# Optimization experiments

Hardware: AMD Instinct MI355X
Metric: run time of the kernel (lower is better)

The kernel has to match this reference:

```python
import jax, jax.numpy as jnp
import numpy as np

TOPK = 8
NUM_EXPERTS = 64


def setup_inputs() -> dict:
    key = jax.random.key(0)
    k0, k1, k2, k3 = jax.random.split(key, 4)
    B, S, H, E = 4, 4096, 2048, NUM_EXPERTS
    scale = (2.0 ** -0.5) * np.sqrt(6.0 / (H + E))  # xavier_uniform gain 2^-0.5
    return {
        "x": jax.random.normal(k0, (B, S, H), dtype=jnp.float32),
        "w_transform": jax.random.uniform(k1, (E, H), jnp.float32, -scale, scale),
        "w_noise": jax.random.uniform(k2, (E, H), jnp.float32, -scale, scale),
        "noise": jax.random.normal(k3, (E,), dtype=jnp.float32),
    }


def reference(x, w_transform, w_noise, noise):
    # weight: [B, S, E]
    logits_t = jnp.einsum("bsh,eh->bse", x, w_transform)
    logits_n = jnp.einsum("bsh,eh->bse", x, w_noise)
    weight = logits_t + jax.nn.softplus(logits_n) * noise  # broadcast noise [E]

    # Global (corpus-level) top-k over expert means
    mean_w = weight.mean(axis=(0, 1))  # [E]
    gates, indexes = jax.lax.top_k(mean_w, TOPK)
    selected_gates = jax.nn.softmax(gates, axis=-1)  # [TOPK]

    # Example-wise top-k -> multi-hot mask [B, S, E]
    _, ew_idx = jax.lax.top_k(weight, TOPK)  # [B, S, TOPK]
    mask = jax.nn.one_hot(ew_idx, NUM_EXPERTS, dtype=weight.dtype).sum(axis=-2) > 0

    # Masked softmax over experts
    masked = jnp.where(mask, weight, -jnp.inf)
    soft_w = jax.nn.softmax(masked, axis=-1)  # [B, S, E]

    # Experts balance loss: (std / mean)^2 of per-expert total weight
    sum_w = soft_w.sum(axis=(0, 1))  # [E]
    cv = jnp.std(sum_w, ddof=1) / jnp.mean(sum_w)  # torch .std() is unbiased
    balance_loss = cv ** 2

    return selected_gates, indexes, balance_loss
```

## Files before the change

### kernel.cpp

```cpp
#include <hip/hip_runtime.h>
#include <math.h>

#define H     2048
#define NE    64
#define KTOP  8
#define NTOK  16384
#define TOKB  64
#define STEPS 32

typedef __attribute__((ext_vector_type(8))) __bf16 bf16x8;
typedef __attribute__((ext_vector_type(8))) unsigned short us8;
typedef __attribute__((ext_vector_type(4))) float f32x4;

__device__ __forceinline__ unsigned short f2bf(float f) {
    unsigned u = __builtin_bit_cast(unsigned, f);
    return (unsigned short)((u + 0x7FFFu + ((u >> 16) & 1u)) >> 16);
}

#define GLOAD_F4(dst, ptr, OFF)                                        \
    asm volatile("global_load_dwordx4 %0, %1, off offset:%2"           \
                 : "=v"(dst) : "v"(ptr), "i"(OFF))
#define WAITV(N)                                                       \
    do { asm volatile("s_waitcnt vmcnt(%0)" :: "i"(N));                \
         __builtin_amdgcn_sched_barrier(0); } while (0)

__global__ __launch_bounds__(256) void k_prep(const float* __restrict__ Wt,
                                              const float* __restrict__ Wn,
                                              unsigned short* __restrict__ wbf2,
                                              float* __restrict__ sums) {
    const int gid = blockIdx.x * 256 + threadIdx.x;
    if (blockIdx.x == 0 && threadIdx.x < 128) sums[threadIdx.x] = 0.f;

    const int ln  = gid & 63;
    const int nb  = (gid >> 6) & 7;
    const int k32 = gid >> 9;
    const int row = nb * 16 + (ln & 15);
    const int col = k32 * 32 + (ln >> 4) * 8;
    const float* src = (row < NE) ? (Wt + (size_t)row * H + col)
                                  : (Wn + (size_t)(row - NE) * H + col);
    float4 v0 = *(const float4*)src;
    float4 v1 = *(const float4*)(src + 4);
    us8 o;
    o[0] = f2bf(v0.x); o[1] = f2bf(v0.y); o[2] = f2bf(v0.z); o[3] = f2bf(v0.w);
    o[4] = f2bf(v1.x); o[5] = f2bf(v1.y); o[6] = f2bf(v1.z); o[7] = f2bf(v1.w);
    *(us8*)(wbf2 + (size_t)gid * 8) = o;
}

__global__ __launch_bounds__(512, 2) void k_main(const float* __restrict__ X,
                                                 const unsigned short* __restrict__ wbf2,
                                                 const float* __restrict__ noise,
                                                 float* __restrict__ sumraw,
                                                 float* __restrict__ sumsoft) {
    __shared__ float cb[4][2048];
    __shared__ float epf[TOKB * 68];
    __shared__ float lsoft[NE];

    const int tid  = threadIdx.x;
    const int wid  = tid >> 6;
    const int lane = tid & 63;
    const int wm   = wid & 3;
    const int kp   = wid >> 2;
    const int lr   = lane & 15;
    const int lg   = lane >> 4;
    const int t0   = blockIdx.x * TOKB;
    const int s0   = (blockIdx.x >> 3) & 31;

    if (tid < NE) lsoft[tid] = 0.f;

    const float* xp = X + (size_t)(t0 + wm * 16 + lr) * H + kp * 1024 + lg * 8;
    const unsigned short* bp0 = wbf2 + (size_t)kp * 32 * 4096 + (size_t)lane * 8;

    f32x4 acc[8];
    #pragma unroll
    for (int i = 0; i < 8; ++i) acc[i] = (f32x4){0.f, 0.f, 0.f, 0.f};

    float4 xb[3][2];
    us8    bb[3][8];

    #define ISSUE(slot, sv)                                                  \
        do {                                                                 \
            const unsigned short* bA = bp0 + (size_t)(sv) * 4096;            \
            const unsigned short* bB = bA + 2048;                            \
            GLOAD_F4(bb[slot][0], bA, 0);                                    \
            GLOAD_F4(bb[slot][1], bA, 1024);                                 \
            GLOAD_F4(bb[slot][2], bA, 2048);                                 \
            GLOAD_F4(bb[slot][3], bA, 3072);                                 \
            GLOAD_F4(bb[slot][4], bB, 0);                                    \
            GLOAD_F4(bb[slot][5], bB, 1024);                                 \
            GLOAD_F4(bb[slot][6], bB, 2048);                                 \
            GLOAD_F4(bb[slot][7], bB, 3072);                                 \
            const float* xA = xp + (size_t)(sv) * 32;                        \
            GLOAD_F4(xb[slot][0], xA, 0);                                    \
            GLOAD_F4(xb[slot][1], xA, 16);                                   \
        } while (0)

    ISSUE(0, (s0 + 0) & 31);
    ISSUE(1, (s0 + 1) & 31);
    ISSUE(2, (s0 + 2) & 31);

    #pragma unroll
    for (int j = 0; j < STEPS; ++j) {
        const int slot = j % 3;
        if (j < STEPS - 2)       WAITV(20);
        else if (j == STEPS - 2) WAITV(10);
        else                     WAITV(0);

        float4 c0 = xb[slot][0], c1 = xb[slot][1];
        bf16x8 af;
        af[0] = (__bf16)c0.x; af[1] = (__bf16)c0.y;
        af[2] = (__bf16)c0.z; af[3] = (__bf16)c0.w;
        af[4] = (__bf16)c1.x; af[5] = (__bf16)c1.y;
        af[6] = (__bf16)c1.z; af[7] = (__bf16)c1.w;
        #pragma unroll
        for (int nb = 0; nb < 8; ++nb) {
            bf16x8 bfr = __builtin_bit_cast(bf16x8, bb[slot][nb]);
            acc[nb] = __builtin_amdgcn_mfma_f32_16x16x32_bf16(af, bfr, acc[nb], 0, 0, 0);
        }
        if (j + 3 < STEPS) ISSUE(slot, (s0 + j + 3) & 31);
    }
    #undef ISSUE

    if (kp == 1) {
        #pragma unroll
        for (int nb = 0; nb < 8; ++nb)
            #pragma unroll
            for (int r = 0; r < 4; ++r)
                cb[wm][(nb * 4 + r) * 64 + lane] = acc[nb][r];
    }
    __syncthreads();

    if (kp == 0) {
        #pragma unroll
        for (int nb = 0; nb < 8; ++nb)
            #pragma unroll
            for (int r = 0; r < 4; ++r)
                acc[nb][r] += cb[wm][(nb * 4 + r) * 64 + lane];
        float nz[4];
        #pragma unroll
        for (int nb = 0; nb < 4; ++nb) nz[nb] = noise[nb * 16 + lr];
        #pragma unroll
        for (int nb = 0; nb < 4; ++nb)
            #pragma unroll
            for (int r = 0; r < 4; ++r) {
                float lt  = acc[nb][r];
                float lnv = acc[nb + 4][r];
                float sp  = fmaxf(lnv, 0.f) + log1pf(expf(-fabsf(lnv)));
                epf[(wm * 16 + lg * 4 + r) * 68 + nb * 16 + lr] = lt + sp * nz[nb];
            }
    }
    __syncthreads();

    if (tid < TOKB) {
        float tv[KTOP]; int ti[KTOP];
        #pragma unroll
        for (int q = 0; q < KTOP; ++q) { tv[q] = -INFINITY; ti[q] = 0; }
        for (int e = 0; e < NE; ++e) {
            float cv = epf[tid * 68 + e]; int ci = e;
            #pragma unroll
            for (int q = 0; q < KTOP; ++q) {
                if (cv > tv[q]) {
                    float t_ = tv[q]; int i_ = ti[q];
                    tv[q] = cv; ti[q] = ci;
                    cv = t_; ci = i_;
                }
            }
        }
        float m = tv[0], den = 0.f, pr[KTOP];
        #pragma unroll
        for (int q = 0; q < KTOP; ++q) { pr[q] = expf(tv[q] - m); den += pr[q]; }
        float inv = 1.f / den;
        #pragma unroll
        for (int q = 0; q < KTOP; ++q) atomicAdd(&lsoft[ti[q]], pr[q] * inv);
    }
    __syncthreads();

    if (tid < NE) {
        float s = 0.f;
        #pragma unroll
        for (int t = 0; t < TOKB; ++t) s += epf[t * 68 + tid];
        atomicAdd(&sumraw[tid], s);
        atomicAdd(&sumsoft[tid], lsoft[tid]);
    }
}

__global__ void k_final(const float* __restrict__ sumraw,
                        const float* __restrict__ sumsoft,
                        float* __restrict__ out) {
    if (threadIdx.x != 0 || blockIdx.x != 0) return;

    float mw[NE];
    for (int e = 0; e < NE; ++e) mw[e] = sumraw[e] * (1.f / (float)NTOK);

    float tv[KTOP]; int ti[KTOP];
    for (int q = 0; q < KTOP; ++q) { tv[q] = -INFINITY; ti[q] = 0; }
    for (int e = 0; e < NE; ++e) {
        float cv = mw[e]; int ci = e;
        for (int q = 0; q < KTOP; ++q) {
            if (cv > tv[q]) {
                float t_ = tv[q]; int i_ = ti[q];
                tv[q] = cv; ti[q] = ci;
                cv = t_; ci = i_;
            }
        }
    }
    float m = tv[0], den = 0.f, pr[KTOP];
    for (int q = 0; q < KTOP; ++q) { pr[q] = expf(tv[q] - m); den += pr[q]; }
    for (int q = 0; q < KTOP; ++q) {
        out[q] = pr[q] / den;
        out[KTOP + q] = (float)ti[q];
    }

    float s = 0.f;
    for (int e = 0; e < NE; ++e) s += sumsoft[e];
    float mean = s / (float)NE;
    float var = 0.f;
    for (int e = 0; e < NE; ++e) { float d = sumsoft[e] - mean; var += d * d; }
    var /= (float)(NE - 1);
    out[16] = var / (mean * mean);
}

extern "C" void kernel_launch(void* const* d_in, const int* in_sizes, int n_in,
                              void* d_out, int out_size, void* d_ws, size_t ws_size,
                              hipStream_t stream) {
    (void)in_sizes; (void)n_in; (void)out_size; (void)ws_size;
    const float* x     = (const float*)d_in[0];
    const float* wt    = (const float*)d_in[1];
    const float* wn    = (const float*)d_in[2];
    const float* noise = (const float*)d_in[3];
    float* out = (float*)d_out;

    float* sumraw  = (float*)d_ws;
    float* sumsoft = sumraw + NE;
    unsigned short* wbf2 = (unsigned short*)(sumsoft + NE);

    k_prep<<<128, 256, 0, stream>>>(wt, wn, wbf2, sumraw);
    k_main<<<256, 512, 0, stream>>>(x, wbf2, noise, sumraw, sumsoft);
    k_final<<<1, 64, 0, stream>>>(sumraw, sumsoft, out);
}
```

Measured before the change: 93.77 us.

## Split experts across block pairs, widen token tile, move top-k to separate kernel

Each main block now computes 128 tokens but only half of the 128 output columns (transform or noise half), so each wave does two M-tiles against four B fragments. This halves the per-wave B loads and doubles A reuse. Logits are written to global memory as bf16, and a new k_topk kernel does softplus, noise mixing, per-token top-k and the reductions, one thread per token. The cost is an extra launch, a logits round trip through memory, bf16 rounding of the logits, and each X row being read by two blocks.

```diff
diff --git a/kernel.cpp b/kernel.cpp
--- a/kernel.cpp
+++ b/kernel.cpp
@@ -5,7 +5,7 @@
 #define NE    64
 #define KTOP  8
 #define NTOK  16384
-#define TOKB  64
+#define TOKB  128
 #define STEPS 32
 
 typedef __attribute__((ext_vector_type(8))) __bf16 bf16x8;
@@ -15,6 +15,9 @@
 __device__ __forceinline__ unsigned short f2bf(float f) {
     unsigned u = __builtin_bit_cast(unsigned, f);
     return (unsigned short)((u + 0x7FFFu + ((u >> 16) & 1u)) >> 16);
+}
+__device__ __forceinline__ float bf2f(unsigned short s) {
+    return __builtin_bit_cast(float, (unsigned)s << 16);
 }
 
 #define GLOAD_F4(dst, ptr, OFF)                                        \
@@ -26,34 +29,31 @@
 
 __global__ __launch_bounds__(256) void k_prep(const float* __restrict__ Wt,
                                               const float* __restrict__ Wn,
-                                              unsigned short* __restrict__ wbf2,
+                                              unsigned short* __restrict__ wbf3,
                                               float* __restrict__ sums) {
     const int gid = blockIdx.x * 256 + threadIdx.x;
     if (blockIdx.x == 0 && threadIdx.x < 128) sums[threadIdx.x] = 0.f;
 
-    const int ln  = gid & 63;
-    const int nb  = (gid >> 6) & 7;
-    const int k32 = gid >> 9;
-    const int row = nb * 16 + (ln & 15);
-    const int col = k32 * 32 + (ln >> 4) * 8;
-    const float* src = (row < NE) ? (Wt + (size_t)row * H + col)
-                                  : (Wn + (size_t)(row - NE) * H + col);
+    const int ln   = gid & 63;
+    const int nb   = (gid >> 6) & 3;
+    const int k32g = (gid >> 8) & 63;
+    const int h    = (gid >> 14) & 1;
+    const int c    = h * 64 + nb * 16 + (ln & 15);
+    const int col  = k32g * 32 + (ln >> 4) * 8;
+    const float* src = (c < NE) ? (Wt + (size_t)c * H + col)
+                                : (Wn + (size_t)(c - NE) * H + col);
     float4 v0 = *(const float4*)src;
     float4 v1 = *(const float4*)(src + 4);
     us8 o;
     o[0] = f2bf(v0.x); o[1] = f2bf(v0.y); o[2] = f2bf(v0.z); o[3] = f2bf(v0.w);
     o[4] = f2bf(v1.x); o[5] = f2bf(v1.y); o[6] = f2bf(v1.z); o[7] = f2bf(v1.w);
-    *(us8*)(wbf2 + (size_t)gid * 8) = o;
+    *(us8*)(wbf3 + (size_t)gid * 8) = o;
 }
 
 __global__ __launch_bounds__(512, 2) void k_main(const float* __restrict__ X,
-                                                 const unsigned short* __restrict__ wbf2,
-                                                 const float* __restrict__ noise,
-                                                 float* __restrict__ sumraw,
-                                                 float* __restrict__ sumsoft) {
+                                                 const unsigned short* __restrict__ wbf3,
+                                                 unsigned short* __restrict__ logits) {
     __shared__ float cb[4][2048];
-    __shared__ float epf[TOKB * 68];
-    __shared__ float lsoft[NE];
 
     const int tid  = threadIdx.x;
     const int wid  = tid >> 6;
@@ -62,123 +62,162 @@
     const int kp   = wid >> 2;
     const int lr   = lane & 15;
     const int lg   = lane >> 4;
-    const int t0   = blockIdx.x * TOKB;
-    const int s0   = (blockIdx.x >> 3) & 31;
-
-    if (tid < NE) lsoft[tid] = 0.f;
-
-    const float* xp = X + (size_t)(t0 + wm * 16 + lr) * H + kp * 1024 + lg * 8;
-    const unsigned short* bp0 = wbf2 + (size_t)kp * 32 * 4096 + (size_t)lane * 8;
-
-    f32x4 acc[8];
-    #pragma unroll
-    for (int i = 0; i < 8; ++i) acc[i] = (f32x4){0.f, 0.f, 0.f, 0.f};
-
-    float4 xb[3][2];
-    us8    bb[3][8];
+    const int blk  = blockIdx.x;
+    const int tt   = blk >> 1;
+    const int h    = blk & 1;
+    const int t0   = tt * TOKB;
+    const int s0   = (blk >> 3) & 31;
+
+    const float* xp0 = X + (size_t)(t0 + wm * 32 + lr) * H + kp * 1024 + lg * 8;
+    const float* xp1 = xp0 + (size_t)16 * H;
+    const unsigned short* bp0 = wbf3 + ((size_t)h * 256 + (size_t)kp * 128) * 512
+                                     + (size_t)lane * 8;
+
+    f32x4 acc[2][4];
+    #pragma unroll
+    for (int m = 0; m < 2; ++m)
+        #pragma unroll
+        for (int i = 0; i < 4; ++i) acc[m][i] = (f32x4){0.f, 0.f, 0.f, 0.f};
+
+    float4 xb[3][2][2];
+    us8    bb[3][4];
 
     #define ISSUE(slot, sv)                                                  \
         do {                                                                 \
-            const unsigned short* bA = bp0 + (size_t)(sv) * 4096;            \
-            const unsigned short* bB = bA + 2048;                            \
+            const unsigned short* bA = bp0 + (size_t)(sv) * 2048;            \
             GLOAD_F4(bb[slot][0], bA, 0);                                    \
             GLOAD_F4(bb[slot][1], bA, 1024);                                 \
             GLOAD_F4(bb[slot][2], bA, 2048);                                 \
             GLOAD_F4(bb[slot][3], bA, 3072);                                 \
-            GLOAD_F4(bb[slot][4], bB, 0);                                    \
-            GLOAD_F4(bb[slot][5], bB, 1024);                                 \
-            GLOAD_F4(bb[slot][6], bB, 2048);                                 \
-            GLOAD_F4(bb[slot][7], bB, 3072);                                 \
-            const float* xA = xp + (size_t)(sv) * 32;                        \
-            GLOAD_F4(xb[slot][0], xA, 0);                                    \
-            GLOAD_F4(xb[slot][1], xA, 16);                                   \
+            const float* xA0 = xp0 + (size_t)(sv) * 32;                      \
+            const float* xA1 = xp1 + (size_t)(sv) * 32;                      \
+            GLOAD_F4(xb[slot][0][0], xA0, 0);                                \
+            GLOAD_F4(xb[slot][0][1], xA0, 16);                               \
+            GLOAD_F4(xb[slot][1][0], xA1, 0);                                \
+            GLOAD_F4(xb[slot][1][1], xA1, 16);                               \
         } while (0)
 
-    ISSUE(0, (s0 + 0) & 31);
+    ISSUE(0, s0);
     ISSUE(1, (s0 + 1) & 31);
     ISSUE(2, (s0 + 2) & 31);
 
     #pragma unroll
     for (int j = 0; j < STEPS; ++j) {
         const int slot = j % 3;
-        if (j < STEPS - 2)       WAITV(20);
-        else if (j == STEPS - 2) WAITV(10);
+        if (j < STEPS - 2)       WAITV(16);
+        else if (j == STEPS - 2) WAITV(8);
         else                     WAITV(0);
 
-        float4 c0 = xb[slot][0], c1 = xb[slot][1];
-        bf16x8 af;
-        af[0] = (__bf16)c0.x; af[1] = (__bf16)c0.y;
-        af[2] = (__bf16)c0.z; af[3] = (__bf16)c0.w;
-        af[4] = (__bf16)c1.x; af[5] = (__bf16)c1.y;
-        af[6] = (__bf16)c1.z; af[7] = (__bf16)c1.w;
-        #pragma unroll
-        for (int nb = 0; nb < 8; ++nb) {
+        bf16x8 af0, af1;
+        {
+            float4 c0 = xb[slot][0][0], c1 = xb[slot][0][1];
+            af0[0] = (__bf16)c0.x; af0[1] = (__bf16)c0.y;
+            af0[2] = (__bf16)c0.z; af0[3] = (__bf16)c0.w;
+            af0[4] = (__bf16)c1.x; af0[5] = (__bf16)c1.y;
+            af0[6] = (__bf16)c1.z; af0[7] = (__bf16)c1.w;
+            float4 d0 = xb[slot][1][0], d1 = xb[slot][1][1];
+            af1[0] = (__bf16)d0.x; af1[1] = (__bf16)d0.y;
+            af1[2] = (__bf16)d0.z; af1[3] = (__bf16)d0.w;
+            af1[4] = (__bf16)d1.x; af1[5] = (__bf16)d1.y;
+            af1[6] = (__bf16)d1.z; af1[7] = (__bf16)d1.w;
+        }
+        #pragma unroll
+        for (int nb = 0; nb < 4; ++nb) {
             bf16x8 bfr = __builtin_bit_cast(bf16x8, bb[slot][nb]);
-            acc[nb] = __builtin_amdgcn_mfma_f32_16x16x32_bf16(af, bfr, acc[nb], 0, 0, 0);
-        }
-        if (j + 3 < STEPS) ISSUE(slot, (s0 + j + 3) & 31);
+            acc[0][nb] = __builtin_amdgcn_mfma_f32_16x16x32_bf16(af0, bfr, acc[0][nb], 0, 0, 0);
+            acc[1][nb] = __builtin_amdgcn_mfma_f32_16x16x32_bf16(af1, bfr, acc[1][nb], 0, 0, 0);
+        }
+        if (j < STEPS - 3) ISSUE(slot, (s0 + j + 3) & 31);
     }
     #undef ISSUE
 
     if (kp == 1) {
         #pragma unroll
-        for (int nb = 0; nb < 8; ++nb)
+        for (int m = 0; m < 2; ++m)
             #pragma unroll
-            for (int r = 0; r < 4; ++r)
-                cb[wm][(nb * 4 + r) * 64 + lane] = acc[nb][r];
+            for (int nb = 0; nb < 4; ++nb)
+                #pragma unroll
+                for (int r = 0; r < 4; ++r)
+                    cb[wm][((m * 4 + nb) * 4 + r) * 64 + lane] = acc[m][nb][r];
     }
     __syncthreads();
-
     if (kp == 0) {
         #pragma unroll
-        for (int nb = 0; nb < 8; ++nb)
+        for (int m = 0; m < 2; ++m)
             #pragma unroll
-            for (int r = 0; r < 4; ++r)
-                acc[nb][r] += cb[wm][(nb * 4 + r) * 64 + lane];
-        float nz[4];
-        #pragma unroll
-        for (int nb = 0; nb < 4; ++nb) nz[nb] = noise[nb * 16 + lr];
-        #pragma unroll
-        for (int nb = 0; nb < 4; ++nb)
-            #pragma unroll
-            for (int r = 0; r < 4; ++r) {
-                float lt  = acc[nb][r];
-                float lnv = acc[nb + 4][r];
-                float sp  = fmaxf(lnv, 0.f) + log1pf(expf(-fabsf(lnv)));
-                epf[(wm * 16 + lg * 4 + r) * 68 + nb * 16 + lr] = lt + sp * nz[nb];
+            for (int nb = 0; nb < 4; ++nb)
+                #pragma unroll
+                for (int r = 0; r < 4; ++r) {
+                    float v = acc[m][nb][r] + cb[wm][((m * 4 + nb) * 4 + r) * 64 + lane];
+                    int tok = t0 + wm * 32 + m * 16 + lg * 4 + r;
+                    int col = h * 64 + nb * 16 + lr;
+                    logits[(size_t)tok * 128 + col] = f2bf(v);
+                }
+    }
+}
+
+__global__ __launch_bounds__(256) void k_topk(const unsigned short* __restrict__ logits,
+                                              const float* __restrict__ noise,
+                                              float* __restrict__ sumraw,
+                                              float* __restrict__ sumsoft) {
+    __shared__ float lsoft[NE];
+    __shared__ float lraw[NE];
+    const int tid = threadIdx.x;
+    const int row = blockIdx.x * 256 + tid;
+
+    if (tid < NE) { lsoft[tid] = 0.f; lraw[tid] = 0.f; }
+    __syncthreads();
+
+    float g[NE];
+    const unsigned short* rp = logits + (size_t)row * 128;
+    #pragma unroll
+    for (int j = 0; j < 8; ++j) {
+        us8 a = *(const us8*)(rp + j * 8);
+        us8 b = *(const us8*)(rp + 64 + j * 8);
+        #pragma unroll
+        for (int q = 0; q < 8; ++q) {
+            int e = j * 8 + q;
+            float lt  = bf2f(a[q]);
+            float lnv = bf2f(b[q]);
+            float sp  = fmaxf(lnv, 0.f) + log1pf(expf(-fabsf(lnv)));
+            g[e] = lt + sp * noise[e];
+        }
+    }
+
+    float tv[KTOP]; int ti[KTOP];
+    #pragma unroll
+    for (int q = 0; q < KTOP; ++q) { tv[q] = -INFINITY; ti[q] = 0; }
+    #pragma unroll
+    for (int e = 0; e < NE; ++e) {
+        float cv = g[e]; int ci = e;
+        #pragma unroll
+        for (int q = 0; q < KTOP; ++q) {
+            if (cv > tv[q]) {
+                float t_ = tv[q]; int i_ = ti[q];
+                tv[q] = cv; ti[q] = ci;
+                cv = t_; ci = i_;
             }
+        }
+    }
+    float m = tv[0], den = 0.f, pr[KTOP];
+    #pragma unroll
+    for (int q = 0; q < KTOP; ++q) { pr[q] = expf(tv[q] - m); den += pr[q]; }
+    float inv = 1.f / den;
+    #pragma unroll
+    for (int q = 0; q < KTOP; ++q) atomicAdd(&lsoft[ti[q]], pr[q] * inv);
+
+    #pragma unroll
+    for (int e = 0; e < NE; ++e) {
+        float v = g[e];
+        v += __shfl_xor(v, 1);  v += __shfl_xor(v, 2);
+        v += __shfl_xor(v, 4);  v += __shfl_xor(v, 8);
+        v += __shfl_xor(v, 16); v += __shfl_xor(v, 32);
+        if ((tid & 63) == 0) atomicAdd(&lraw[e], v);
     }
     __syncthreads();
 
-    if (tid < TOKB) {
-        float tv[KTOP]; int ti[KTOP];
-        #pragma unroll
-        for (int q = 0; q < KTOP; ++q) { tv[q] = -INFINITY; ti[q] = 0; }
-        for (int e = 0; e < NE; ++e) {
-            float cv = epf[tid * 68 + e]; int ci = e;
-            #pragma unroll
-            for (int q = 0; q < KTOP; ++q) {
-                if (cv > tv[q]) {
-                    float t_ = tv[q]; int i_ = ti[q];
-                    tv[q] = cv; ti[q] = ci;
-                    cv = t_; ci = i_;
-                }
-            }
-        }
-        float m = tv[0], den = 0.f, pr[KTOP];
-        #pragma unroll
-        for (int q = 0; q < KTOP; ++q) { pr[q] = expf(tv[q] - m); den += pr[q]; }
-        float inv = 1.f / den;
-        #pragma unroll
-        for (int q = 0; q < KTOP; ++q) atomicAdd(&lsoft[ti[q]], pr[q] * inv);
-    }
-    __syncthreads();
-
     if (tid < NE) {
-        float s = 0.f;
-        #pragma unroll
-        for (int t = 0; t < TOKB; ++t) s += epf[t * 68 + tid];
-        atomicAdd(&sumraw[tid], s);
+        atomicAdd(&sumraw[tid], lraw[tid]);
         atomicAdd(&sumsoft[tid], lsoft[tid]);
     }
 }
@@ -231,9 +270,11 @@
 
     float* sumraw  = (float*)d_ws;
     float* sumsoft = sumraw + NE;
-    unsigned short* wbf2 = (unsigned short*)(sumsoft + NE);
-
-    k_prep<<<128, 256, 0, stream>>>(wt, wn, wbf2, sumraw);
-    k_main<<<256, 512, 0, stream>>>(x, wbf2, noise, sumraw, sumsoft);
+    unsigned short* wbf3   = (unsigned short*)(sumsoft + NE);
+    unsigned short* logits = wbf3 + (size_t)512 * 512;
+
+    k_prep<<<128, 256, 0, stream>>>(wt, wn, wbf3, sumraw);
+    k_main<<<256, 512, 0, stream>>>(x, wbf3, logits);
+    k_topk<<<64, 256, 0, stream>>>(logits, noise, sumraw, sumsoft);
     k_final<<<1, 64, 0, stream>>>(sumraw, sumsoft, out);
 }
```

Result: slower. 138.9 us (+48.2%).

## Give each wave two 16-row M tiles to reuse weight fragments

Applied to the files above, without the earlier changes.

Halves the block to 256 threads (4 waves) and makes each wave compute 32 token rows instead of 16, so each loaded bf16 weight fragment feeds two MFMAs. This cuts the weight load traffic per token in half. In exchange it doubles the accumulator and X-prefetch registers per wave and leaves fewer waves per block to hide latency. The launch bounds drop to one block per 256 threads, which permits higher register use.

```diff
diff --git a/kernel.cpp b/kernel.cpp
--- a/kernel.cpp
+++ b/kernel.cpp
@@ -46,20 +46,20 @@
     *(us8*)(wbf2 + (size_t)gid * 8) = o;
 }
 
-__global__ __launch_bounds__(512, 2) void k_main(const float* __restrict__ X,
+__global__ __launch_bounds__(256, 1) void k_main(const float* __restrict__ X,
                                                  const unsigned short* __restrict__ wbf2,
                                                  const float* __restrict__ noise,
                                                  float* __restrict__ sumraw,
                                                  float* __restrict__ sumsoft) {
-    __shared__ float cb[4][2048];
+    __shared__ float cb[2][4096];
     __shared__ float epf[TOKB * 68];
     __shared__ float lsoft[NE];
 
     const int tid  = threadIdx.x;
     const int wid  = tid >> 6;
     const int lane = tid & 63;
-    const int wm   = wid & 3;
-    const int kp   = wid >> 2;
+    const int wm   = wid & 1;
+    const int kp   = wid >> 1;
     const int lr   = lane & 15;
     const int lg   = lane >> 4;
     const int t0   = blockIdx.x * TOKB;
@@ -67,14 +67,17 @@
 
     if (tid < NE) lsoft[tid] = 0.f;
 
-    const float* xp = X + (size_t)(t0 + wm * 16 + lr) * H + kp * 1024 + lg * 8;
+    const float* xp0 = X + (size_t)(t0 + wm * 32 + lr) * H + kp * 1024 + lg * 8;
+    const float* xp1 = xp0 + (size_t)16 * H;
     const unsigned short* bp0 = wbf2 + (size_t)kp * 32 * 4096 + (size_t)lane * 8;
 
-    f32x4 acc[8];
+    f32x4 acc[2][8];
     #pragma unroll
-    for (int i = 0; i < 8; ++i) acc[i] = (f32x4){0.f, 0.f, 0.f, 0.f};
-
-    float4 xb[3][2];
+    for (int m = 0; m < 2; ++m)
+        #pragma unroll
+        for (int i = 0; i < 8; ++i) acc[m][i] = (f32x4){0.f, 0.f, 0.f, 0.f};
+
+    float4 xb[3][2][2];
     us8    bb[3][8];
 
     #define ISSUE(slot, sv)                                                  \
@@ -89,32 +92,43 @@
             GLOAD_F4(bb[slot][5], bB, 1024);                                 \
             GLOAD_F4(bb[slot][6], bB, 2048);                                 \
             GLOAD_F4(bb[slot][7], bB, 3072);                                 \
-            const float* xA = xp + (size_t)(sv) * 32;                        \
-            GLOAD_F4(xb[slot][0], xA, 0);                                    \
-            GLOAD_F4(xb[slot][1], xA, 16);                                   \
+            const float* xA0 = xp0 + (size_t)(sv) * 32;                      \
+            const float* xA1 = xp1 + (size_t)(sv) * 32;                      \
+            GLOAD_F4(xb[slot][0][0], xA0, 0);                                \
+            GLOAD_F4(xb[slot][0][1], xA0, 16);                               \
+            GLOAD_F4(xb[slot][1][0], xA1, 0);                                \
+            GLOAD_F4(xb[slot][1][1], xA1, 16);                               \
         } while (0)
 
-    ISSUE(0, (s0 + 0) & 31);
+    ISSUE(0, s0);
     ISSUE(1, (s0 + 1) & 31);
     ISSUE(2, (s0 + 2) & 31);
 
     #pragma unroll
     for (int j = 0; j < STEPS; ++j) {
         const int slot = j % 3;
-        if (j < STEPS - 2)       WAITV(20);
-        else if (j == STEPS - 2) WAITV(10);
+        if (j < STEPS - 2)       WAITV(24);
+        else if (j == STEPS - 2) WAITV(12);
         else                     WAITV(0);
 
-        float4 c0 = xb[slot][0], c1 = xb[slot][1];
-        bf16x8 af;
-        af[0] = (__bf16)c0.x; af[1] = (__bf16)c0.y;
-        af[2] = (__bf16)c0.z; af[3] = (__bf16)c0.w;
-        af[4] = (__bf16)c1.x; af[5] = (__bf16)c1.y;
-        af[6] = (__bf16)c1.z; af[7] = (__bf16)c1.w;
+        bf16x8 af0, af1;
+        {
+            float4 c0 = xb[slot][0][0], c1 = xb[slot][0][1];
+            af0[0] = (__bf16)c0.x; af0[1] = (__bf16)c0.y;
+            af0[2] = (__bf16)c0.z; af0[3] = (__bf16)c0.w;
+            af0[4] = (__bf16)c1.x; af0[5] = (__bf16)c1.y;
+            af0[6] = (__bf16)c1.z; af0[7] = (__bf16)c1.w;
+            float4 d0 = xb[slot][1][0], d1 = xb[slot][1][1];
+            af1[0] = (__bf16)d0.x; af1[1] = (__bf16)d0.y;
+            af1[2] = (__bf16)d0.z; af1[3] = (__bf16)d0.w;
+            af1[4] = (__bf16)d1.x; af1[5] = (__bf16)d1.y;
+            af1[6] = (__bf16)d1.z; af1[7] = (__bf16)d1.w;
+        }
         #pragma unroll
         for (int nb = 0; nb < 8; ++nb) {
             bf16x8 bfr = __builtin_bit_cast(bf16x8, bb[slot][nb]);
-            acc[nb] = __builtin_amdgcn_mfma_f32_16x16x32_bf16(af, bfr, acc[nb], 0, 0, 0);
+            acc[0][nb] = __builtin_amdgcn_mfma_f32_16x16x32_bf16(af0, bfr, acc[0][nb], 0, 0, 0);
+            acc[1][nb] = __builtin_amdgcn_mfma_f32_16x16x32_bf16(af1, bfr, acc[1][nb], 0, 0, 0);
         }
         if (j + 3 < STEPS) ISSUE(slot, (s0 + j + 3) & 31);
     }
@@ -122,31 +136,37 @@
 
     if (kp == 1) {
         #pragma unroll
-        for (int nb = 0; nb < 8; ++nb)
-            #pragma unroll
-            for (int r = 0; r < 4; ++r)
-                cb[wm][(nb * 4 + r) * 64 + lane] = acc[nb][r];
+        for (int m = 0; m < 2; ++m)
+            #pragma unroll
+            for (int nb = 0; nb < 8; ++nb)
+                #pragma unroll
+                for (int r = 0; r < 4; ++r)
+                    cb[wm][((m * 8 + nb) * 4 + r) * 64 + lane] = acc[m][nb][r];
     }
     __syncthreads();
 
     if (kp == 0) {
         #pragma unroll
-        for (int nb = 0; nb < 8; ++nb)
-            #pragma unroll
-            for (int r = 0; r < 4; ++r)
-                acc[nb][r] += cb[wm][(nb * 4 + r) * 64 + lane];
+        for (int m = 0; m < 2; ++m)
+            #pragma unroll
+            for (int nb = 0; nb < 8; ++nb)
+                #pragma unroll
+                for (int r = 0; r < 4; ++r)
+                    acc[m][nb][r] += cb[wm][((m * 8 + nb) * 4 + r) * 64 + lane];
         float nz[4];
         #pragma unroll
         for (int nb = 0; nb < 4; ++nb) nz[nb] = noise[nb * 16 + lr];
         #pragma unroll
-        for (int nb = 0; nb < 4; ++nb)
-            #pragma unroll
-            for (int r = 0; r < 4; ++r) {
-                float lt  = acc[nb][r];
-                float lnv = acc[nb + 4][r];
-                float sp  = fmaxf(lnv, 0.f) + log1pf(expf(-fabsf(lnv)));
-                epf[(wm * 16 + lg * 4 + r) * 68 + nb * 16 + lr] = lt + sp * nz[nb];
-            }
+        for (int m = 0; m < 2; ++m)
+            #pragma unroll
+            for (int nb = 0; nb < 4; ++nb)
+                #pragma unroll
+                for (int r = 0; r < 4; ++r) {
+                    float lt  = acc[m][nb][r];
+                    float lnv = acc[m][nb + 4][r];
+                    float sp  = fmaxf(lnv, 0.f) + log1pf(expf(-fabsf(lnv)));
+                    epf[(wm * 32 + m * 16 + lg * 4 + r) * 68 + nb * 16 + lr] = lt + sp * nz[nb];
+                }
     }
     __syncthreads();
 
@@ -234,6 +254,6 @@
     unsigned short* wbf2 = (unsigned short*)(sumsoft + NE);
 
     k_prep<<<128, 256, 0, stream>>>(wt, wn, wbf2, sumraw);
-    k_main<<<256, 512, 0, stream>>>(x, wbf2, noise, sumraw, sumsoft);
+    k_main<<<256, 256, 0, stream>>>(x, wbf2, noise, sumraw, sumsoft);
     k_final<<<1, 64, 0, stream>>>(sumraw, sumsoft, out);
 }
```

Measured after the change: 99.69 us. +6.3%, slower.
